# Optimization experiments

Measured on AMD Instinct MI355X. Metric: run time of the kernel, lower is better.

## Reference

```python
import jax, jax.numpy as jnp
import numpy as np

V = [8192, 2048, 512, 128, 32]   # vertex counts per mesh level
S = 9                            # spiral length
T = 64                           # number of audio frames
OC = [32, 64, 64, 128]           # out_channels
LAT = 64                         # latent_channels


def _spiral_conv(x, idx, w, b):
    # x: [B, Vi, C], idx: [Vi, S] -> gather spiral neighborhoods, flatten, linear
    B = x.shape[0]
    n, s = idx.shape
    g = x[:, idx.reshape(-1), :].reshape(B, n, -1)  # [B, Vi, S*C]
    return g @ w + b


def _pool(x, row, col, val, out_size):
    # sparse COO matmul along vertex dim: out[b, r, :] += val * x[b, c, :]
    g = x[:, col, :] * val[None, :, None]
    return jnp.zeros((x.shape[0], out_size, x.shape[2]), x.dtype).at[:, row, :].add(g)


def setup_inputs():
    key = jax.random.key(0)
    keys = iter(jax.random.split(key, 80))
    def nrm(shape, scale=0.05):
        return jax.random.normal(next(keys), shape, jnp.float32) * scale
    inp = {}
    inp["hidden_states"] = jax.random.normal(next(keys), (1, T, 768), jnp.float32)
    inp["actor"] = jax.random.normal(next(keys), (1, V[0], 3), jnp.float32)
    inp["audio_w"] = nrm((768, LAT)); inp["audio_b"] = jnp.zeros((LAT,), jnp.float32)
    enc_dims = [(3 * S, OC[0]), (OC[0] * S, OC[1]), (OC[1] * S, OC[2]), (OC[2] * S, OC[3])]
    for i, (a, b) in enumerate(enc_dims):
        inp[f"enc{i}_w"] = nrm((a, b)); inp[f"enc{i}_b"] = jnp.zeros((b,), jnp.float32)
    inp["enc_lat_w"] = nrm((V[4] * OC[3], LAT)); inp["enc_lat_b"] = jnp.zeros((LAT,), jnp.float32)
    inp["dec_lin_w"] = nrm((2 * LAT, V[4] * OC[3])); inp["dec_lin_b"] = jnp.zeros((V[4] * OC[3],), jnp.float32)
    dec_dims = [(OC[3] * S, OC[3]), (OC[3] * S, OC[2]), (OC[2] * S, OC[1]), (OC[1] * S, OC[0])]
    for i, (a, b) in enumerate(dec_dims):
        inp[f"dec{i}_w"] = nrm((a, b)); inp[f"dec{i}_b"] = jnp.zeros((b,), jnp.float32)
    inp["dec_out_w"] = nrm((OC[0] * S, 3)); inp["dec_out_b"] = jnp.zeros((3,), jnp.float32)
    for i in range(4):
        inp[f"spiral{i}"] = jax.random.randint(next(keys), (V[i], S), 0, V[i])
    for i in range(4):
        vin, vout = V[i], V[i + 1]
        inp[f"down{i}_row"] = jnp.repeat(jnp.arange(vout), 3)
        inp[f"down{i}_col"] = jax.random.randint(next(keys), (3 * vout,), 0, vin)
        inp[f"down{i}_val"] = jax.random.uniform(next(keys), (3 * vout,), jnp.float32) / 3.0
        inp[f"up{i}_row"] = jnp.repeat(jnp.arange(vin), 3)
        inp[f"up{i}_col"] = jax.random.randint(next(keys), (3 * vin,), 0, vout)
        inp[f"up{i}_val"] = jax.random.uniform(next(keys), (3 * vin,), jnp.float32) / 3.0
    return inp


def reference(hidden_states, actor, audio_w, audio_b,
              enc0_w, enc0_b, enc1_w, enc1_b, enc2_w, enc2_b, enc3_w, enc3_b,
              enc_lat_w, enc_lat_b,
              dec_lin_w, dec_lin_b, dec0_w, dec0_b, dec1_w, dec1_b,
              dec2_w, dec2_b, dec3_w, dec3_b, dec_out_w, dec_out_b,
              spiral0, spiral1, spiral2, spiral3,
              down0_row, down0_col, down0_val, down1_row, down1_col, down1_val,
              down2_row, down2_col, down2_val, down3_row, down3_col, down3_val,
              up0_row, up0_col, up0_val, up1_row, up1_col, up1_val,
              up2_row, up2_col, up2_val, up3_row, up3_col, up3_val):
    spirals = [spiral0, spiral1, spiral2, spiral3]
    enc_p = [(enc0_w, enc0_b), (enc1_w, enc1_b), (enc2_w, enc2_b), (enc3_w, enc3_b)]
    dec_p = [(dec0_w, dec0_b), (dec1_w, dec1_b), (dec2_w, dec2_b), (dec3_w, dec3_b)]
    down = [(down0_row, down0_col, down0_val), (down1_row, down1_col, down1_val),
            (down2_row, down2_col, down2_val), (down3_row, down3_col, down3_val)]
    up = [(up0_row, up0_col, up0_val), (up1_row, up1_col, up1_val),
          (up2_row, up2_col, up2_val), (up3_row, up3_col, up3_val)]

    # ---- encode(actor): conv -> elu -> pool per level, then flatten linear ----
    x = actor  # [1, V0, 3]
    for i in range(4):
        w, b = enc_p[i]
        x = jax.nn.elu(_spiral_conv(x, spirals[i], w, b))
        r, c, v = down[i]
        x = _pool(x, r, c, v, V[i + 1])
    actor_emb = x.reshape(1, -1) @ enc_lat_w + enc_lat_b  # [1, LAT]

    # ---- audio embedding and latent concat ----
    audio_emb = hidden_states[0] @ audio_w + audio_b       # [T, LAT]
    latent = jnp.concatenate(
        [audio_emb, jnp.broadcast_to(actor_emb, audio_emb.shape)], axis=-1)  # [T, 2*LAT]

    # ---- decode all frames at once (original loops per frame; batched over T) ----
    x = (latent @ dec_lin_w + dec_lin_b).reshape(-1, V[4], OC[3])  # [T, V4, OC3]
    for i in range(4):
        lvl = 3 - i
        r, c, v = up[lvl]
        x = _pool(x, r, c, v, V[lvl])
        w, b = dec_p[i]
        x = jax.nn.elu(_spiral_conv(x, spirals[lvl], w, b))
    x = _spiral_conv(x, spirals[0], dec_out_w, dec_out_b)  # [T, V0, 3]
    return x + actor  # broadcast actor (displacement prediction), pred_sequence[1:]
```

## Files before the change

### kernel.cpp

```cpp
#include <hip/hip_runtime.h>
#include <hip/hip_bf16.h>

typedef __hip_bfloat16 bf16;
typedef __attribute__((ext_vector_type(8))) short short8v;
typedef __attribute__((ext_vector_type(16))) float f32x16;

__device__ __forceinline__ float tof(float v){ return v; }
__device__ __forceinline__ float tof(bf16 v){ return __bfloat162float(v); }
__device__ __forceinline__ void sto(float* p, float v){ *p = v; }
__device__ __forceinline__ void sto(bf16* p, float v){ *p = __float2bfloat16(v); }
__device__ __forceinline__ short f2bs(float f){ bf16 h = __float2bfloat16(f); return *(short*)&h; }
__device__ __forceinline__ float bsu2f(short s){
    return __uint_as_float(((unsigned)(unsigned short)s) << 16);
}

__device__ __forceinline__ void sto4(float* p, float4 v){ *(float4*)p = v; }
__device__ __forceinline__ void sto4(bf16* p, float4 v){
    short4 s; s.x=f2bs(v.x); s.y=f2bs(v.y); s.z=f2bs(v.z); s.w=f2bs(v.w);
    *(short4*)p = s;
}

__device__ __forceinline__ void swz_t(int b, int bs, int& t, int& rem){
    int x = b & 7, k = b >> 3;
    t = x*8 + (k >> bs);
    rem = k & ((1 << bs) - 1);
}

__global__ __launch_bounds__(256) void k_prep(
    const float* __restrict__ w0, const float* __restrict__ w1,
    const float* __restrict__ w2, const float* __restrict__ w3,
    const float* __restrict__ w4,
    short* __restrict__ wt0, short* __restrict__ wt1,
    short* __restrict__ wt2, short* __restrict__ wt3,
    short* __restrict__ wt4,
    const float* __restrict__ hs, const float* __restrict__ aw,
    const float* __restrict__ ab, float* __restrict__ aemb)
{
    __shared__ float red[4][64];
    int b = blockIdx.x, tid = threadIdx.x;
    if (b < 1080){
        const float* w; short* wt; int K, nsh, i;
        if      (b < 576) { w = w0; wt = wt0; K = 1152; nsh = 7; i = b*256 + tid; }
        else if (b < 864) { w = w1; wt = wt1; K = 1152; nsh = 6; i = (b-576)*256 + tid; }
        else if (b < 1008){ w = w2; wt = wt2; K = 576;  nsh = 6; i = (b-864)*256 + tid; }
        else              { w = w3; wt = wt3; K = 576;  nsh = 5; i = (b-1008)*256 + tid; }
        int k = i >> nsh, n = i & ((1 << nsh) - 1);
        wt[n*K + k] = f2bs(w[i]);
    } else if (b < 1116){
        int i = (b - 1080)*256 + tid;
        int k = i >> 5, n = i & 31;
        wt4[n*288 + k] = (n < 3) ? f2bs(w4[k*3 + n]) : (short)0;
    } else {
        int t = b - 1116;
        int kg = tid >> 6, l = tid & 63;
        const float* h = hs + t*768;
        float acc = 0.f;
        int k0 = kg*192;
        #pragma unroll 8
        for (int k = k0; k < k0 + 192; k++) acc += h[k] * aw[k*64 + l];
        red[kg][l] = acc;
        __syncthreads();
        if (kg == 0)
            aemb[t*64 + l] = red[0][l] + red[1][l] + red[2][l] + red[3][l] + ab[l];
    }
}

__global__ __launch_bounds__(256) void k_enclat(const float* __restrict__ flat,
    const float* __restrict__ w, const float* __restrict__ b, float* __restrict__ out)
{
    __shared__ float red[256];
    int l = blockIdx.x, tid = threadIdx.x;
    float acc = 0.f;
    for (int k = tid; k < 4096; k += 256) acc += flat[k] * w[k*64 + l];
    red[tid] = acc; __syncthreads();
    for (int s = 128; s > 0; s >>= 1){ if (tid < s) red[tid] += red[tid+s]; __syncthreads(); }
    if (tid == 0) out[l] = red[0] + b[l];
}

__global__ __launch_bounds__(256) void k_declin4(const float* __restrict__ ae,
    const float* __restrict__ pe, const float* __restrict__ w, const float* __restrict__ b,
    bf16* __restrict__ out)
{
    int n4 = blockIdx.x*256 + threadIdx.x;
    int t = blockIdx.y;
    float4 acc = *(const float4*)&b[n4*4];
    const float* a = ae + t*64;
    #pragma unroll 4
    for (int k = 0; k < 64; k++){
        float av = a[k];
        float4 wv = *(const float4*)&w[(size_t)k*4096 + n4*4];
        acc.x += av*wv.x; acc.y += av*wv.y; acc.z += av*wv.z; acc.w += av*wv.w;
    }
    #pragma unroll 4
    for (int k = 0; k < 64; k++){
        float pv = pe[k];
        float4 wv = *(const float4*)&w[(size_t)(64+k)*4096 + n4*4];
        acc.x += pv*wv.x; acc.y += pv*wv.y; acc.z += pv*wv.z; acc.w += pv*wv.w;
    }
    sto4(&out[(size_t)t*4096 + n4*4], acc);
}

__global__ __launch_bounds__(256) void k_pool4(const float* __restrict__ xin,
    const int* __restrict__ col, const float* __restrict__ val, float* __restrict__ out,
    int total4, int c4mask, int cs, int vomask, int vos, int Vi)
{
    int i = blockIdx.x*256 + threadIdx.x;
    if (i >= total4) return;
    int c4 = i & c4mask;
    int rv = i >> cs;
    int r  = rv & vomask;
    int t  = rv >> vos;
    int C  = (c4mask + 1) << 2;
    const float* xt = xin + (size_t)t * Vi * C;
    int r3 = 3*r;
    int j0 = col[r3], j1 = col[r3+1], j2 = col[r3+2];
    float v0 = val[r3], v1 = val[r3+1], v2 = val[r3+2];
    int c = c4 << 2;
    float4 a = *(const float4*)&xt[(size_t)j0*C + c];
    float4 b = *(const float4*)&xt[(size_t)j1*C + c];
    float4 d = *(const float4*)&xt[(size_t)j2*C + c];
    float4 o;
    o.x = v0*a.x + v1*b.x + v2*d.x;
    o.y = v0*a.y + v1*b.y + v2*d.y;
    o.z = v0*a.z + v1*b.z + v2*d.z;
    o.w = v0*a.w + v1*b.w + v2*d.w;
    sto4(&out[(size_t)i << 2], o);
}

__global__ __launch_bounds__(256) void k_poolb(const bf16* __restrict__ xin,
    const int* __restrict__ col, const float* __restrict__ val, bf16* __restrict__ out,
    int c8mask, int cs, int vom, int vshin, int cshift, int bs, int ept8)
{
    int t, rem; swz_t(blockIdx.x, bs, t, rem);
    int il = rem*256 + threadIdx.x;
    int c8 = il & c8mask;
    int r  = (il >> cs) & vom;
    size_t i = (size_t)t * ept8 + il;
    const bf16* xt = xin + ((size_t)t << (vshin + cshift));
    int r3 = 3*r;
    int j0 = col[r3], j1 = col[r3+1], j2 = col[r3+2];
    float v0 = val[r3], v1 = val[r3+1], v2 = val[r3+2];
    int c = c8 << 3;
    short8v a = *(const short8v*)&xt[((size_t)j0 << cshift) + c];
    short8v b = *(const short8v*)&xt[((size_t)j1 << cshift) + c];
    short8v d = *(const short8v*)&xt[((size_t)j2 << cshift) + c];
    short8v o;
    #pragma unroll
    for (int q = 0; q < 8; q++)
        o[q] = f2bs(v0*bsu2f(a[q]) + v1*bsu2f(b[q]) + v2*bsu2f(d[q]));
    *(short8v*)&out[i << 3] = o;
}

template<int KTOT, int CSHIFT, int NTOT, typename TOUT>
__global__ __launch_bounds__(256) void k_conv_p3(
    const bf16* __restrict__ xin, const int* __restrict__ spiral,
    const short* __restrict__ wt, const float* __restrict__ bias, TOUT* __restrict__ out,
    int vshift, int bs, int nbshift)
{
    constexpr int NCH  = KTOT >> 6;
    constexpr int CSUB = CSHIFT - 6;
    __shared__ short lds_a[2*128*72];
    __shared__ short lds_b[2*32*72];
    const int tid = threadIdx.x;
    const int lane = tid & 63;
    const int wv = tid >> 6;
    const int col = lane & 31;
    const int half = lane >> 5;

    int t, rem; swz_t(blockIdx.x, bs, t, rem);
    const int nb = rem & ((1 << nbshift) - 1);
    const int vt = rem >> nbshift;
    const int mbase = vt*128;
    const size_t xslab = (size_t)t << (vshift + CSHIFT);

    const int am = tid >> 3;
    const int ak = (tid & 7) << 3;
    const int bn = tid >> 3;
    const int bk = (tid & 7) << 3;

    short8v pa[3][4];
    short8v pb[3];

    auto issue = [&](int ch, int st){
        int s = ch >> CSUB;
        int coff = ((ch & ((1 << CSUB) - 1)) << 6) + ak;
        #pragma unroll
        for (int u = 0; u < 4; u++){
            int j = spiral[(mbase + am + u*32)*9 + s];
            pa[st][u] = *(const short8v*)&xin[xslab + ((size_t)j << CSHIFT) + coff];
        }
        pb[st] = *(const short8v*)&wt[(size_t)(nb*32 + bn)*KTOT + (ch << 6) + bk];
    };
    auto commit = [&](int ch, int st){
        short* la = lds_a + (ch & 1)*(128*72);
        short* lb = lds_b + (ch & 1)*(32*72);
        #pragma unroll
        for (int u = 0; u < 4; u++)
            *(short8v*)&la[(am + u*32)*72 + ak] = pa[st][u];
        *(short8v*)&lb[bn*72 + bk] = pb[st];
    };

    f32x16 acc;
    {
        float bv = bias[nb*32 + col];
        #pragma unroll
        for (int r = 0; r < 16; r++) acc[r] = bv;
    }

    issue(0, 0);
    issue(1, 1);
    issue(2, 2);
    commit(0, 0);
    __syncthreads();
    for (int ch = 0; ch < NCH; ch++){
        if (ch + 3 < NCH) issue(ch + 3, ch % 3);
        const short* la = lds_a + (ch & 1)*(128*72);
        const short* lb = lds_b + (ch & 1)*(32*72);
        #pragma unroll
        for (int ks = 0; ks < 4; ks++){
            short8v b = *(const short8v*)&lb[col*72 + ks*16 + half*8];
            short8v a = *(const short8v*)&la[(wv*32 + col)*72 + ks*16 + half*8];
            acc = __builtin_amdgcn_mfma_f32_32x32x16_bf16(a, b, acc, 0, 0, 0);
        }
        if (ch + 1 < NCH) commit(ch + 1, (ch + 1) % 3);
        __syncthreads();
    }
    size_t mb = ((size_t)t << vshift) + mbase + wv*32;
    #pragma unroll
    for (int r = 0; r < 16; r++){
        int row = (r & 3) + 8*(r >> 2) + 4*half;
        float vv = acc[r];
        vv = vv > 0.f ? vv : __expf(vv) - 1.f;
        sto(&out[(mb + row)*NTOT + nb*32 + col], vv);
    }
}

__global__ __launch_bounds__(256) void k_outmfma(
    const bf16* __restrict__ xin, const int* __restrict__ spiral,
    const short* __restrict__ wt, const float* __restrict__ bias,
    const float* __restrict__ actor, float* __restrict__ out)
{
    __shared__ short lds_a[2*256*36];
    __shared__ short lds_b[2*32*36];
    const int tid = threadIdx.x;
    const int lane = tid & 63;
    const int wv = tid >> 6;
    const int col = lane & 31;
    const int half = lane >> 5;

    int t, rem; swz_t(blockIdx.x, 5, t, rem);
    const int mbase = rem*256;
    const size_t xslab = (size_t)t << 18;

    short8v pa[3][4];
    short8v pb[3];
    const int am = tid >> 2;
    const int ak = (tid & 3) << 3;

    auto issue = [&](int s, int st){
        #pragma unroll
        for (int u = 0; u < 4; u++){
            int j = spiral[(mbase + am + u*64)*9 + s];
            pa[st][u] = *(const short8v*)&xin[xslab + ((size_t)j << 5) + ak];
        }
        if (tid < 128)
            pb[st] = *(const short8v*)&wt[am*288 + s*32 + ak];
    };
    auto commit = [&](int s, int st){
        short* la = lds_a + (s & 1)*(256*36);
        short* lb = lds_b + (s & 1)*(32*36);
        #pragma unroll
        for (int u = 0; u < 4; u++)
            *(short8v*)&la[(am + u*64)*36 + ak] = pa[st][u];
        if (tid < 128)
            *(short8v*)&lb[am*36 + ak] = pb[st];
    };

    f32x16 acc[2];
    {
        float bv = (col < 3) ? bias[col] : 0.f;
        #pragma unroll
        for (int h = 0; h < 2; h++)
            #pragma unroll
            for (int r = 0; r < 16; r++) acc[h][r] = bv;
    }

    issue(0, 0);
    issue(1, 1);
    issue(2, 2);
    commit(0, 0);
    __syncthreads();
    for (int s = 0; s < 9; s++){
        if (s + 3 < 9) issue(s + 3, s % 3);
        const short* la = lds_a + (s & 1)*(256*36);
        const short* lb = lds_b + (s & 1)*(32*36);
        #pragma unroll
        for (int ks = 0; ks < 2; ks++){
            short8v b = *(const short8v*)&lb[col*36 + ks*16 + half*8];
            #pragma unroll
            for (int h = 0; h < 2; h++){
                short8v a = *(const short8v*)&la[(h*128 + wv*32 + col)*36 + ks*16 + half*8];
                acc[h] = __builtin_amdgcn_mfma_f32_32x32x16_bf16(a, b, acc[h], 0, 0, 0);
            }
        }
        if (s + 1 < 9) commit(s + 1, (s + 1) % 3);
        __syncthreads();
    }
    if (col < 3){
        #pragma unroll
        for (int h = 0; h < 2; h++){
            int rowb = mbase + h*128 + wv*32;
            #pragma unroll
            for (int r = 0; r < 16; r++){
                int row = rowb + (r & 3) + 8*(r >> 2) + 4*half;
                out[(((size_t)t << 13) + row)*3 + col] = acc[h][r] + actor[row*3 + col];
            }
        }
    }
}

template<typename TIN>
__global__ __launch_bounds__(256) void k_conv(const TIN* __restrict__ xin,
    const int* __restrict__ spiral, const float* __restrict__ w, const float* __restrict__ bias,
    float* __restrict__ out, int TV, int V, int vshift, int C, int O2, int o2shift,
    int K, int KP, int MT)
{
    extern __shared__ float lds[];
    const int S = 9;
    int tid = threadIdx.x;
    int O = O2 << 1;
    int gmbase = blockIdx.x * MT;

    int total = MT * K;
    for (int e = tid; e < total; e += 256){
        int m = e / K, k = e - m*K;
        int gm = gmbase + m;
        if (gm < TV){
            int t = gm >> vshift, v = gm & (V-1);
            int s = k / C, c = k - s*C;
            int jj = spiral[v*S + s];
            lds[m*KP + k] = tof(xin[((size_t)t*V + jj)*C + c]);
        }
    }
    __syncthreads();

    int m = tid >> o2shift;
    int o = tid & (O2 - 1);
    int gm = gmbase + m;
    if (gm >= TV) return;
    const float* g  = lds + m*KP;
    const float* wp = w + 2*o;
    float acc0 = bias[2*o];
    float acc1 = bias[2*o+1];
    int K4 = K & ~3;
    for (int k = 0; k < K4; k += 4){
        float4 g4 = *(const float4*)(g + k);
        float2 w0 = *(const float2*)(wp + (size_t)k    *O);
        float2 w1 = *(const float2*)(wp + (size_t)(k+1)*O);
        float2 w2 = *(const float2*)(wp + (size_t)(k+2)*O);
        float2 w3 = *(const float2*)(wp + (size_t)(k+3)*O);
        acc0 += g4.x*w0.x + g4.y*w1.x + g4.z*w2.x + g4.w*w3.x;
        acc1 += g4.x*w0.y + g4.y*w1.y + g4.z*w2.y + g4.w*w3.y;
    }
    for (int k = K4; k < K; k++){
        float gv = g[k];
        acc0 += gv * wp[(size_t)k*O];
        acc1 += gv * wp[(size_t)k*O + 1];
    }
    acc0 = acc0 > 0.f ? acc0 : __expf(acc0) - 1.f;
    acc1 = acc1 > 0.f ? acc1 : __expf(acc1) - 1.f;
    float2 r; r.x = acc0; r.y = acc1;
    *(float2*)(out + (size_t)gm*O + 2*o) = r;
}

extern "C" void kernel_launch(void* const* d_in, const int* in_sizes, int n_in,
                              void* d_out, int out_size, void* d_ws, size_t ws_size,
                              hipStream_t stream)
{
    (void)n_in; (void)out_size; (void)ws_size;
    const float* hs        = (const float*)d_in[0];
    const float* actor     = (const float*)d_in[1];
    const float* audio_w   = (const float*)d_in[2];
    const float* audio_b   = (const float*)d_in[3];
    const float* enc_w[4]  = {(const float*)d_in[4],(const float*)d_in[6],(const float*)d_in[8],(const float*)d_in[10]};
    const float* enc_b[4]  = {(const float*)d_in[5],(const float*)d_in[7],(const float*)d_in[9],(const float*)d_in[11]};
    const float* enc_lat_w = (const float*)d_in[12];
    const float* enc_lat_b = (const float*)d_in[13];
    const float* dec_lin_w = (const float*)d_in[14];
    const float* dec_lin_b = (const float*)d_in[15];
    const float* dec_w[4]  = {(const float*)d_in[16],(const float*)d_in[18],(const float*)d_in[20],(const float*)d_in[22]};
    const float* dec_b[4]  = {(const float*)d_in[17],(const float*)d_in[19],(const float*)d_in[21],(const float*)d_in[23]};
    const float* dec_out_w = (const float*)d_in[24];
    const float* dec_out_b = (const float*)d_in[25];
    const int*   spiral[4] = {(const int*)d_in[26],(const int*)d_in[27],(const int*)d_in[28],(const int*)d_in[29]};

    const int* dcol[4]; const float* dval[4]; const int* ucol[4]; const float* uval[4];
    bool interleaved = (in_sizes[33] == 3*8192);
    for (int i = 0; i < 4; i++){
        if (interleaved){
            int b = 30 + 6*i;
            dcol[i] = (const int*)d_in[b+1]; dval[i] = (const float*)d_in[b+2];
            ucol[i] = (const int*)d_in[b+4]; uval[i] = (const float*)d_in[b+5];
        } else {
            dcol[i] = (const int*)d_in[31+3*i]; dval[i] = (const float*)d_in[32+3*i];
            ucol[i] = (const int*)d_in[43+3*i]; uval[i] = (const float*)d_in[44+3*i];
        }
    }

    char* ws = (char*)d_ws;
    size_t off = 0;
    auto alloc = [&](size_t bytes)->char* {
        char* p = ws + off; off += (bytes + 255) & ~(size_t)255; return p;
    };
    float* encX0 = (float*)alloc((size_t)262144*4);
    float* encP0 = (float*)alloc((size_t)65536*4);
    float* encX1 = (float*)alloc((size_t)131072*4);
    float* encP1 = (float*)alloc((size_t)32768*4);
    float* encX2 = (float*)alloc((size_t)32768*4);
    float* encP2 = (float*)alloc((size_t)8192*4);
    float* encX3 = (float*)alloc((size_t)16384*4);
    float* encP3 = (float*)alloc((size_t)4096*4);
    float* aemb  = (float*)alloc((size_t)4096*4);
    float* pemb  = (float*)alloc((size_t)64*4);
    short* wt0   = (short*)alloc((size_t)147456*2);
    short* wt1   = (short*)alloc((size_t)73728*2);
    short* wt2   = (short*)alloc((size_t)36864*2);
    short* wt3   = (short*)alloc((size_t)18432*2);
    short* wt4   = (short*)alloc((size_t)9216*2);
    bf16*  Pb    = (bf16*)alloc((size_t)36*1048576);
    bf16*  Qb    = (bf16*)alloc((size_t)68*1048576);

    k_prep<<<1180,256,0,stream>>>(dec_w[0], dec_w[1], dec_w[2], dec_w[3], dec_out_w,
                                  wt0, wt1, wt2, wt3, wt4, hs, audio_w, audio_b, aemb);

    k_conv<float><<<512,256, 16*28*4, stream>>>(actor, spiral[0], enc_w[0], enc_b[0], encX0, 8192, 8192,13,   3,16,4,  27,  28,16);
    k_pool4<<<64,256,0,stream>>>(encX0, dcol[0], dval[0], encP0, 16384, 7,3, 2047,11, 8192);
    k_conv<float><<<256,256, 8*292*4, stream>>>(encP0, spiral[1], enc_w[1], enc_b[1], encX1, 2048, 2048,11,  32,32,5, 288, 292, 8);
    k_pool4<<<32,256,0,stream>>>(encX1, dcol[1], dval[1], encP1, 8192, 15,4, 511,9, 2048);
    k_conv<float><<<64,256, 8*580*4, stream>>>(encP1, spiral[2], enc_w[2], enc_b[2], encX2, 512, 512,9,  64,32,5, 576, 580, 8);
    k_pool4<<<8,256,0,stream>>>(encX2, dcol[2], dval[2], encP2, 2048, 15,4, 127,7, 512);
    k_conv<float><<<32,256, 4*580*4, stream>>>(encP2, spiral[3], enc_w[3], enc_b[3], encX3, 128, 128,7,  64,64,6, 576, 580, 4);
    k_pool4<<<4,256,0,stream>>>(encX3, dcol[3], dval[3], encP3, 1024, 31,5, 31,5, 128);
    k_enclat<<<64,256,0,stream>>>(encP3, enc_lat_w, enc_lat_b, pemb);

    k_declin4<<<dim3(4,64),256,0,stream>>>(aemb, pemb, dec_lin_w, dec_lin_b, Pb);

    k_poolb<<<512,256,0,stream>>>(Pb, ucol[3], uval[3], Qb, 15,4, 127, 5,7, 3, 2048);
    k_conv_p3<1152,7,128,bf16><<<256,256,0,stream>>>(Qb, spiral[3], wt0, dec_b[0], Pb, 7, 2, 2);

    k_poolb<<<2048,256,0,stream>>>(Pb, ucol[2], uval[2], Qb, 15,4, 511, 7,7, 5, 8192);
    k_conv_p3<1152,7,64,bf16><<<512,256,0,stream>>>(Qb, spiral[2], wt1, dec_b[1], Pb, 9, 3, 1);

    k_poolb<<<4096,256,0,stream>>>(Pb, ucol[1], uval[1], Qb, 7,3, 2047, 9,6, 6, 16384);
    k_conv_p3<576,6,64,bf16><<<2048,256,0,stream>>>(Qb, spiral[1], wt2, dec_b[2], Pb, 11, 5, 1);

    k_poolb<<<16384,256,0,stream>>>(Pb, ucol[0], uval[0], Qb, 7,3, 8191, 11,6, 8, 65536);
    k_conv_p3<576,6,32,bf16><<<4096,256,0,stream>>>(Qb, spiral[0], wt3, dec_b[3], Pb, 13, 6, 0);

    k_outmfma<<<2048,256,0,stream>>>(Pb, spiral[0], wt4, dec_out_b, actor, (float*)d_out);
}
```

Measured before the change: 497.4 us.

## Fuse encoder down-pooling into following spiral conv and latent linear

Removes the four separate encoder pool kernels by computing the 3-term sparse pooling inline while gathering the spiral neighbourhood in the next conv and in the latent linear. This saves four launches and the intermediate pooled buffers. In exchange the pooled values are recomputed redundantly, about nine times per vertex plus once per output column in the latent kernel. Separately, it adds full unrolling to the pipelined MFMA chunk loops in the decoder conv kernels.

```diff
diff --git a/kernel.cpp b/kernel.cpp
--- a/kernel.cpp
+++ b/kernel.cpp
@@ -65,13 +65,21 @@
     }
 }
 
-__global__ __launch_bounds__(256) void k_enclat(const float* __restrict__ flat,
+__global__ __launch_bounds__(256) void k_enclat_f(const float* __restrict__ X3,
+    const int* __restrict__ col, const float* __restrict__ val,
     const float* __restrict__ w, const float* __restrict__ b, float* __restrict__ out)
 {
     __shared__ float red[256];
     int l = blockIdx.x, tid = threadIdx.x;
     float acc = 0.f;
-    for (int k = tid; k < 4096; k += 256) acc += flat[k] * w[k*64 + l];
+    for (int k = tid; k < 4096; k += 256){
+        int j = k >> 7, c = k & 127;
+        int r3 = 3*j;
+        float p = val[r3  ] * X3[col[r3  ]*128 + c]
+                + val[r3+1] * X3[col[r3+1]*128 + c]
+                + val[r3+2] * X3[col[r3+2]*128 + c];
+        acc += p * w[k*64 + l];
+    }
     red[tid] = acc; __syncthreads();
     for (int s = 128; s > 0; s >>= 1){ if (tid < s) red[tid] += red[tid+s]; __syncthreads(); }
     if (tid == 0) out[l] = red[0] + b[l];
@@ -98,33 +106,6 @@
         acc.x += pv*wv.x; acc.y += pv*wv.y; acc.z += pv*wv.z; acc.w += pv*wv.w;
     }
     sto4(&out[(size_t)t*4096 + n4*4], acc);
-}
-
-__global__ __launch_bounds__(256) void k_pool4(const float* __restrict__ xin,
-    const int* __restrict__ col, const float* __restrict__ val, float* __restrict__ out,
-    int total4, int c4mask, int cs, int vomask, int vos, int Vi)
-{
-    int i = blockIdx.x*256 + threadIdx.x;
-    if (i >= total4) return;
-    int c4 = i & c4mask;
-    int rv = i >> cs;
-    int r  = rv & vomask;
-    int t  = rv >> vos;
-    int C  = (c4mask + 1) << 2;
-    const float* xt = xin + (size_t)t * Vi * C;
-    int r3 = 3*r;
-    int j0 = col[r3], j1 = col[r3+1], j2 = col[r3+2];
-    float v0 = val[r3], v1 = val[r3+1], v2 = val[r3+2];
-    int c = c4 << 2;
-    float4 a = *(const float4*)&xt[(size_t)j0*C + c];
-    float4 b = *(const float4*)&xt[(size_t)j1*C + c];
-    float4 d = *(const float4*)&xt[(size_t)j2*C + c];
-    float4 o;
-    o.x = v0*a.x + v1*b.x + v2*d.x;
-    o.y = v0*a.y + v1*b.y + v2*d.y;
-    o.z = v0*a.z + v1*b.z + v2*d.z;
-    o.w = v0*a.w + v1*b.w + v2*d.w;
-    sto4(&out[(size_t)i << 2], o);
 }
 
 __global__ __launch_bounds__(256) void k_poolb(const bf16* __restrict__ xin,
@@ -212,6 +193,7 @@
     issue(2, 2);
     commit(0, 0);
     __syncthreads();
+    #pragma unroll
     for (int ch = 0; ch < NCH; ch++){
         if (ch + 3 < NCH) issue(ch + 3, ch % 3);
         const short* la = lds_a + (ch & 1)*(128*72);
@@ -290,6 +272,7 @@
     issue(2, 2);
     commit(0, 0);
     __syncthreads();
+    #pragma unroll
     for (int s = 0; s < 9; s++){
         if (s + 3 < 9) issue(s + 3, s % 3);
         const short* la = lds_a + (s & 1)*(256*36);
@@ -319,14 +302,12 @@
     }
 }
 
-template<typename TIN>
-__global__ __launch_bounds__(256) void k_conv(const TIN* __restrict__ xin,
+__global__ __launch_bounds__(256) void k_conv(const float* __restrict__ xin,
     const int* __restrict__ spiral, const float* __restrict__ w, const float* __restrict__ bias,
-    float* __restrict__ out, int TV, int V, int vshift, int C, int O2, int o2shift,
+    float* __restrict__ out, int TV, int C, int O2, int o2shift,
     int K, int KP, int MT)
 {
     extern __shared__ float lds[];
-    const int S = 9;
     int tid = threadIdx.x;
     int O = O2 << 1;
     int gmbase = blockIdx.x * MT;
@@ -336,10 +317,9 @@
         int m = e / K, k = e - m*K;
         int gm = gmbase + m;
         if (gm < TV){
-            int t = gm >> vshift, v = gm & (V-1);
             int s = k / C, c = k - s*C;
-            int jj = spiral[v*S + s];
-            lds[m*KP + k] = tof(xin[((size_t)t*V + jj)*C + c]);
+            int jj = spiral[gm*9 + s];
+            lds[m*KP + k] = xin[(size_t)jj*C + c];
         }
     }
     __syncthreads();
@@ -373,6 +353,62 @@
     *(float2*)(out + (size_t)gm*O + 2*o) = r;
 }
 
+__global__ __launch_bounds__(256) void k_convf(const float* __restrict__ xin,
+    const int* __restrict__ spiral, const int* __restrict__ pcol, const float* __restrict__ pval,
+    const float* __restrict__ w, const float* __restrict__ bias,
+    float* __restrict__ out, int TV, int C, int O2, int o2shift,
+    int K, int KP, int MT)
+{
+    extern __shared__ float lds[];
+    int tid = threadIdx.x;
+    int O = O2 << 1;
+    int gmbase = blockIdx.x * MT;
+
+    int total = MT * K;
+    for (int e = tid; e < total; e += 256){
+        int m = e / K, k = e - m*K;
+        int gm = gmbase + m;
+        if (gm < TV){
+            int s = k / C, c = k - s*C;
+            int j = spiral[gm*9 + s];
+            int r3 = 3*j;
+            float p = pval[r3  ] * xin[(size_t)pcol[r3  ]*C + c]
+                    + pval[r3+1] * xin[(size_t)pcol[r3+1]*C + c]
+                    + pval[r3+2] * xin[(size_t)pcol[r3+2]*C + c];
+            lds[m*KP + k] = p;
+        }
+    }
+    __syncthreads();
+
+    int m = tid >> o2shift;
+    int o = tid & (O2 - 1);
+    int gm = gmbase + m;
+    if (gm >= TV) return;
+    const float* g  = lds + m*KP;
+    const float* wp = w + 2*o;
+    float acc0 = bias[2*o];
+    float acc1 = bias[2*o+1];
+    int K4 = K & ~3;
+    for (int k = 0; k < K4; k += 4){
+        float4 g4 = *(const float4*)(g + k);
+        float2 w0 = *(const float2*)(wp + (size_t)k    *O);
+        float2 w1 = *(const float2*)(wp + (size_t)(k+1)*O);
+        float2 w2 = *(const float2*)(wp + (size_t)(k+2)*O);
+        float2 w3 = *(const float2*)(wp + (size_t)(k+3)*O);
+        acc0 += g4.x*w0.x + g4.y*w1.x + g4.z*w2.x + g4.w*w3.x;
+        acc1 += g4.x*w0.y + g4.y*w1.y + g4.z*w2.y + g4.w*w3.y;
+    }
+    for (int k = K4; k < K; k++){
+        float gv = g[k];
+        acc0 += gv * wp[(size_t)k*O];
+        acc1 += gv * wp[(size_t)k*O + 1];
+    }
+    acc0 = acc0 > 0.f ? acc0 : __expf(acc0) - 1.f;
+    acc1 = acc1 > 0.f ? acc1 : __expf(acc1) - 1.f;
+    float2 r; r.x = acc0; r.y = acc1;
+    *(float2*)(out + (size_t)gm*O + 2*o) = r;
+}
+
 extern "C" void kernel_launch(void* const* d_in, const int* in_sizes, int n_in,
                               void* d_out, int out_size, void* d_ws, size_t ws_size,
                               hipStream_t stream)
@@ -413,13 +449,9 @@
         char* p = ws + off; off += (bytes + 255) & ~(size_t)255; return p;
     };
     float* encX0 = (float*)alloc((size_t)262144*4);
-    float* encP0 = (float*)alloc((size_t)65536*4);
     float* encX1 = (float*)alloc((size_t)131072*4);
-    float* encP1 = (float*)alloc((size_t)32768*4);
     float* encX2 = (float*)alloc((size_t)32768*4);
-    float* encP2 = (float*)alloc((size_t)8192*4);
     float* encX3 = (float*)alloc((size_t)16384*4);
-    float* encP3 = (float*)alloc((size_t)4096*4);
     float* aemb  = (float*)alloc((size_t)4096*4);
     float* pemb  = (float*)alloc((size_t)64*4);
     short* wt0   = (short*)alloc((size_t)147456*2);
@@ -433,15 +465,15 @@
     k_prep<<<1180,256,0,stream>>>(dec_w[0], dec_w[1], dec_w[2], dec_w[3], dec_out_w,
                                   wt0, wt1, wt2, wt3, wt4, hs, audio_w, audio_b, aemb);
 
-    k_conv<float><<<512,256, 16*28*4, stream>>>(actor, spiral[0], enc_w[0], enc_b[0], encX0, 8192, 8192,13,   3,16,4,  27,  28,16);
-    k_pool4<<<64,256,0,stream>>>(encX0, dcol[0], dval[0], encP0, 16384, 7,3, 2047,11, 8192);
-    k_conv<float><<<256,256, 8*292*4, stream>>>(encP0, spiral[1], enc_w[1], enc_b[1], encX1, 2048, 2048,11,  32,32,5, 288, 292, 8);
-    k_pool4<<<32,256,0,stream>>>(encX1, dcol[1], dval[1], encP1, 8192, 15,4, 511,9, 2048);
-    k_conv<float><<<64,256, 8*580*4, stream>>>(encP1, spiral[2], enc_w[2], enc_b[2], encX2, 512, 512,9,  64,32,5, 576, 580, 8);
-    k_pool4<<<8,256,0,stream>>>(encX2, dcol[2], dval[2], encP2, 2048, 15,4, 127,7, 512);
-    k_conv<float><<<32,256, 4*580*4, stream>>>(encP2, spiral[3], enc_w[3], enc_b[3], encX3, 128, 128,7,  64,64,6, 576, 580, 4);
-    k_pool4<<<4,256,0,stream>>>(encX3, dcol[3], dval[3], encP3, 1024, 31,5, 31,5, 128);
-    k_enclat<<<64,256,0,stream>>>(encP3, enc_lat_w, enc_lat_b, pemb);
+    k_conv<<<512,256, 16*28*4, stream>>>(actor, spiral[0], enc_w[0], enc_b[0], encX0,
+                                         8192, 3,16,4, 27, 28,16);
+    k_convf<<<256,256, 8*292*4, stream>>>(encX0, spiral[1], dcol[0], dval[0], enc_w[1], enc_b[1], encX1,
+                                          2048, 32,32,5, 288, 292, 8);
+    k_convf<<<64,256, 8*580*4, stream>>>(encX1, spiral[2], dcol[1], dval[1], enc_w[2], enc_b[2], encX2,
+                                         512, 64,32,5, 576, 580, 8);
+    k_convf<<<32,256, 4*580*4, stream>>>(encX2, spiral[3], dcol[2], dval[2], enc_w[3], enc_b[3], encX3,
+                                         128, 64,64,6, 576, 580, 4);
+    k_enclat_f<<<64,256,0,stream>>>(encX3, dcol[3], dval[3], enc_lat_w, enc_lat_b, pemb);
 
     k_declin4<<<dim3(4,64),256,0,stream>>>(aemb, pemb, dec_lin_w, dec_lin_b, Pb);
 
```

After: 497.8 us. Within noise of the previous version (+0.1%).
